# Kernel tuning notes

Hardware: AMD Instinct MI355X
Metric: run time of the kernel (lower is better)

Reference implementation:

```python
import jax, jax.numpy as jnp
import numpy as np

EPS = 1e-5
DN = ('NCHW', 'OIHW', 'NCHW')

def _conv(x, w):
    return jax.lax.conv_general_dilated(x, w, (1, 1), 'VALID', dimension_numbers=DN)

def _bn4(x, g, b, m, v):
    # BatchNorm2d in eval mode, per-channel over NCHW
    inv = g / jnp.sqrt(v + EPS)
    return x * inv[None, :, None, None] + (b - m * inv)[None, :, None, None]

def _bn1(x, g, b, m, v):
    inv = g / jnp.sqrt(v + EPS)
    return x * inv[None, :] + (b - m * inv)[None, :]

def _hardtanh(x):
    return jnp.clip(x, -1.0, 1.0)

def _sign(x):
    return jnp.sign(x)

def _maxpool2(x):
    return jax.lax.reduce_window(x, -jnp.inf, jax.lax.max,
                                 (1, 1, 2, 2), (1, 1, 2, 2), 'VALID')

def setup_inputs() -> dict:
    key = jax.random.key(0)
    ks = jax.random.split(key, 20)
    B = 8192
    d = {
        'x': jax.random.normal(ks[0], (B, 8, 16, 16), jnp.float32),
        'w0': jax.random.normal(ks[1], (32, 8, 3, 3), jnp.float32) * 0.1,
        'b0': jax.random.normal(ks[2], (32,), jnp.float32) * 0.1,
        'g1': jax.random.uniform(ks[3], (32,), jnp.float32, 0.5, 1.5),
        'be1': jax.random.normal(ks[4], (32,), jnp.float32) * 0.1,
        'm1': jax.random.normal(ks[5], (32,), jnp.float32) * 0.1,
        'v1': jax.random.uniform(ks[6], (32,), jnp.float32, 0.5, 1.5),
        'w2': jax.random.normal(ks[7], (32, 32, 3, 3), jnp.float32) * 0.1,
        'g2': jax.random.uniform(ks[8], (32,), jnp.float32, 0.5, 1.5),
        'be2': jax.random.normal(ks[9], (32,), jnp.float32) * 0.1,
        'm2': jax.random.normal(ks[10], (32,), jnp.float32) * 0.1,
        'v2': jax.random.uniform(ks[11], (32,), jnp.float32, 0.5, 1.5),
        'w_fc': jax.random.normal(ks[12], (516, 1152), jnp.float32) * 0.03,
        'g3': jax.random.uniform(ks[13], (516,), jnp.float32, 0.5, 1.5),
        'be3': jax.random.normal(ks[14], (516,), jnp.float32) * 0.1,
        'm3': jax.random.normal(ks[15], (516,), jnp.float32) * 0.1,
        'v3': jax.random.uniform(ks[16], (516,), jnp.float32, 0.5, 1.5),
        'w_last': jax.random.normal(ks[17], (10, 516), jnp.float32) * 0.05,
        'b_last': jax.random.normal(ks[18], (10,), jnp.float32) * 0.05,
    }
    return d

def reference(x, w0, b0, g1, be1, m1, v1, w2, g2, be2, m2, v2,
              w_fc, g3, be3, m3, v3, w_last, b_last):
    # initial float conv + BN + Hardtanh
    h = _conv(x, w0) + b0[None, :, None, None]          # [B,32,14,14]
    h = _hardtanh(_bn4(h, g1, be1, m1, v1))
    # binarized conv (sign(input), sign(weight), no bias)
    h = _conv(_sign(h), _sign(w2))                      # [B,32,12,12]
    h = _hardtanh(_bn4(h, g2, be2, m2, v2))
    h = _maxpool2(h)                                    # [B,32,6,6]
    # dropout is identity in eval mode
    h = h.reshape(h.shape[0], -1)                       # [B,1152]
    # binarized linear (no bias)
    h = _sign(h) @ _sign(w_fc).T                        # [B,516]
    h = _hardtanh(_bn1(h, g3, be3, m3, v3))
    return h @ w_last.T + b_last[None, :]               # [B,10]
```

## Files before the change

### kernel.cpp

```cpp
#include <hip/hip_runtime.h>
#include <cstdint>

#define EPSF 1e-5f

typedef __attribute__((ext_vector_type(8))) short short8;
typedef __attribute__((ext_vector_type(4))) float f32x4;
typedef __attribute__((ext_vector_type(4))) unsigned int u32x4;

__device__ inline uint32_t bf16rne(float x) {
    uint32_t u = __builtin_bit_cast(uint32_t, x);
    return (u + 0x7fffu + ((u >> 16) & 1u)) >> 16;
}
__device__ inline float bf16f(uint32_t b) {
    return __builtin_bit_cast(float, b << 16);
}

__global__ __launch_bounds__(256) void prep_kernel(
    const float* __restrict__ w2, const float* __restrict__ wfc,
    const float* __restrict__ g3, const float* __restrict__ be3,
    const float* __restrict__ m3, const float* __restrict__ v3,
    const float* __restrict__ wlast,
    const float* __restrict__ w0, const float* __restrict__ b0,
    const float* __restrict__ g1, const float* __restrict__ be1,
    const float* __restrict__ m1, const float* __restrict__ v1,
    const float* __restrict__ g2, const float* __restrict__ be2,
    const float* __restrict__ m2, const float* __restrict__ v2,
    uint32_t* __restrict__ w2bits, uint32_t* __restrict__ wfcb,
    float* __restrict__ inv3p, float* __restrict__ sh3p, float* __restrict__ wlt,
    uint32_t* __restrict__ bfrag, float2* __restrict__ bn1c,
    float2* __restrict__ bn1r, int* __restrict__ ti2)
{
    int id = blockIdx.x * 256 + threadIdx.x;
    if (id < 288) {
        int co = id / 9, r = id % 9;
        uint32_t b = 0;
        for (int ci = 0; ci < 32; ci++)
            b |= (uint32_t)(w2[(co * 32 + ci) * 9 + r] < 0.f) << ci;
        w2bits[id] = b;
        return;
    }
    id -= 288;
    if (id < 36 * 576) {
        int j = id / 36, pos = id % 36;
        uint32_t b = 0;
        if (j < 516) {
            const float* row = wfc + j * 1152 + pos;
            for (int c = 0; c < 32; c++)
                b |= (uint32_t)(row[c * 36] < 0.f) << c;
        }
        wfcb[pos * 576 + j] = b;
        return;
    }
    id -= 36 * 576;
    if (id < 576) {
        float iv = 0.f, sh = 0.f;
        if (id < 516) {
            iv = g3[id] / sqrtf(__fadd_rn(v3[id], EPSF));
            sh = __fsub_rn(be3[id], __fmul_rn(m3[id], iv));
        }
        inv3p[id] = iv; sh3p[id] = sh;
        return;
    }
    id -= 576;
    if (id < 5760) {
        int k = id / 576, j = id % 576;
        wlt[id] = (j < 516) ? wlast[k * 516 + j] : 0.f;
        return;
    }
    id -= 5760;
    if (id < 768) {
        int L = id / 12, r = id % 12;
        int nt = r / 6, s = (r % 6) / 2, h = r & 1;
        int g = L >> 4, n = L & 15;
        int tap = 4 * s + g;
        uint32_t d[4] = {0, 0, 0, 0};
        if (tap < 9) {
            int co = nt * 16 + n;
            for (int j2 = 0; j2 < 4; j2++) {
                float wa = w0[co * 72 + (2 * j2) * 9 + tap];
                float wb = w0[co * 72 + (2 * j2 + 1) * 9 + tap];
                uint32_t ha = bf16rne(wa), hb = bf16rne(wb);
                uint32_t va, vb;
                if (h == 0) { va = ha; vb = hb; }
                else { va = bf16rne(wa - bf16f(ha)); vb = bf16rne(wb - bf16f(hb)); }
                d[j2] = va | (vb << 16);
            }
        }
        *(u32x4*)(bfrag + id * 4) = (u32x4){d[0], d[1], d[2], d[3]};
        return;
    }
    id -= 768;
    if (id < 32) {
        float iv = g1[id] / sqrtf(__fadd_rn(v1[id], EPSF));
        float sh = __fsub_rn(be1[id], __fmul_rn(m1[id], iv));
        float off = __fadd_rn(__fmul_rn(b0[id], iv), sh);
        double thrd = -(double)off / (double)iv;
        float thr = (float)thrd;
        float mm = (float)(3.2e-4 / (double)iv + fabs(thrd) * 2e-7 + 1e-9);
        bn1c[id] = make_float2(thr, mm);
        bn1r[id] = make_float2(iv, off);
        return;
    }
    id -= 32;
    if (id < 32) {
        float ivv = g2[id] / sqrtf(__fadd_rn(v2[id], EPSF));
        float shv = __fsub_rn(be2[id], __fmul_rn(m2[id], ivv));
        int M = -290;
        for (int mx = -288; mx <= 288; mx += 2)
            if (__fadd_rn(__fmul_rn((float)mx, ivv), shv) < 0.f) M = mx;
        ti2[id] = (288 - M) >> 1;
    }
}

__device__ __noinline__ bool recheck_sign(const float* __restrict__ xim,
                                          const float* __restrict__ w0,
                                          int py, int px, int co,
                                          const float2* __restrict__ bn1r)
{
    double ad = 0.0;
    for (int ci = 0; ci < 8; ci++)
        for (int ky = 0; ky < 3; ky++)
            for (int kx = 0; kx < 3; kx++)
                ad = fma((double)xim[ci * 256 + (py + ky) * 16 + px + kx],
                         (double)w0[co * 72 + ci * 9 + ky * 3 + kx], ad);
    float2 cc = bn1r[co];
    return (ad * (double)cc.x + (double)cc.y) < 0.0;
}

__global__ __launch_bounds__(128, 4) void convAB(
    const float* __restrict__ x, const float* __restrict__ w0,
    const uint32_t* __restrict__ bfrag, const float2* __restrict__ bn1c,
    const float2* __restrict__ bn1r,
    const uint32_t* __restrict__ w2bits, const int* __restrict__ ti2,
    uint32_t* __restrict__ fcin)
{
    __shared__ __align__(16) char simg[9216];
    __shared__ __align__(8) uint32_t s1l[196];

    const int t = threadIdx.x;
    const int wv = t >> 6, lane = t & 63;
    const int img = blockIdx.x;
    const float* xim = x + img * 2048;
    char* hib = simg;
    char* lob = simg + 4608;

    const int g = lane >> 4;
    const int n = lane & 15;

    short8 Bh[2][3], Bl[2][3];
    {
        const uint32_t* bb = bfrag + lane * 48;
        #pragma unroll
        for (int nt = 0; nt < 2; nt++)
            #pragma unroll
            for (int s = 0; s < 3; s++) {
                Bh[nt][s] = *(const short8*)(bb + (nt * 6 + s * 2) * 4);
                Bl[nt][s] = *(const short8*)(bb + (nt * 6 + s * 2 + 1) * 4);
            }
    }
    const float2 bnA = bn1c[n], bnB = bn1c[16 + n];

    #pragma unroll
    for (int qq = 0; qq < 2; qq++) {
        int pos = lane + 64 * (2 * wv + qq);
        uint32_t hw[4], lw[4];
        #pragma unroll
        for (int j2 = 0; j2 < 4; j2++) {
            float a = xim[(2 * j2) * 256 + pos];
            float b = xim[(2 * j2 + 1) * 256 + pos];
            uint32_t ha = bf16rne(a), hb = bf16rne(b);
            uint32_t la = bf16rne(a - bf16f(ha)), lb = bf16rne(b - bf16f(hb));
            hw[j2] = ha | (hb << 16);
            lw[j2] = la | (lb << 16);
        }
        *(u32x4*)(hib + pos * 16) = (u32x4){hw[0], hw[1], hw[2], hw[3]};
        *(u32x4*)(lob + pos * 16) = (u32x4){lw[0], lw[1], lw[2], lw[3]};
    }
    if (lane < 32) {
        char* gp = (wv == 0) ? hib : lob;
        *(u32x4*)(gp + (256 + lane) * 16) = (u32x4){0, 0, 0, 0};
    }

    int koff[3];
    #pragma unroll
    for (int s = 0; s < 3; s++) {
        int tap = 4 * s + g;
        koff[s] = (tap < 9) ? ((tap / 3) * 16 + (tap % 3)) * 16 : 0;
    }

    __syncthreads();

    for (int tile = wv; tile < 13; tile += 2) {
        int posA = tile * 16 + n;
        int pyA = posA / 14, pxA = posA - pyA * 14;
        int sl = (pyA * 16 + pxA) * 16;

        f32x4 acc0 = {0.f, 0.f, 0.f, 0.f}, acc1 = {0.f, 0.f, 0.f, 0.f};
        #pragma unroll
        for (int s = 0; s < 3; s++) {
            short8 Ah = *(const short8*)(hib + sl + koff[s]);
            short8 Al = *(const short8*)(lob + sl + koff[s]);
            acc0 = __builtin_amdgcn_mfma_f32_16x16x32_bf16(Al, Bh[0][s], acc0, 0, 0, 0);
            acc0 = __builtin_amdgcn_mfma_f32_16x16x32_bf16(Ah, Bl[0][s], acc0, 0, 0, 0);
            acc0 = __builtin_amdgcn_mfma_f32_16x16x32_bf16(Ah, Bh[0][s], acc0, 0, 0, 0);
            acc1 = __builtin_amdgcn_mfma_f32_16x16x32_bf16(Al, Bh[1][s], acc1, 0, 0, 0);
            acc1 = __builtin_amdgcn_mfma_f32_16x16x32_bf16(Ah, Bl[1][s], acc1, 0, 0, 0);
            acc1 = __builtin_amdgcn_mfma_f32_16x16x32_bf16(Ah, Bh[1][s], acc1, 0, 0, 0);
        }

        #pragma unroll
        for (int r = 0; r < 4; r++) {
            int pos = tile * 16 + 4 * g + r;
            float d0 = acc0[r] - bnA.x;
            float d1 = acc1[r] - bnB.x;
            bool bit0, bit1;
            if (__builtin_expect(pos < 196 && fabsf(d0) < bnA.y, 0)) {
                int py = pos / 14, px = pos - py * 14;
                bit0 = recheck_sign(xim, w0, py, px, n, bn1r);
            } else bit0 = (d0 < 0.f);
            if (__builtin_expect(pos < 196 && fabsf(d1) < bnB.y, 0)) {
                int py = pos / 14, px = pos - py * 14;
                bit1 = recheck_sign(xim, w0, py, px, 16 + n, bn1r);
            } else bit1 = (d1 < 0.f);
            unsigned long long m0 = __ballot(bit0);
            unsigned long long m1 = __ballot(bit1);
            uint32_t word = (uint32_t)((m0 >> (16 * g)) & 0xffffull)
                          | ((uint32_t)((m1 >> (16 * g)) & 0xffffull) << 16);
            if (n == 0 && pos < 196) s1l[pos] = word;
        }
    }

    __syncthreads();

    {
        const int c = lane & 31, h = lane >> 5;
        uint32_t wr[9];
        #pragma unroll
        for (int k = 0; k < 9; k++) wr[k] = w2bits[c * 9 + k];
        const int ti = ti2[c];
        uint32_t* outp = fcin + img * 36;
        const int cb0 = 6 * h;

        for (int yy = 0; yy < 3; yy++) {
            const int y2 = 3 * wv + yy;
            const int rbase = 2 * y2 * 14;
            uint32_t win[4][4];
            #pragma unroll
            for (int rr = 0; rr < 4; rr++) {
                uint2 a = *(const uint2*)&s1l[rbase + rr * 14 + cb0];
                uint2 b = *(const uint2*)&s1l[rbase + rr * 14 + cb0 + 2];
                win[rr][0] = a.x; win[rr][1] = a.y; win[rr][2] = b.x; win[rr][3] = b.y;
            }
            for (int step = 0; step < 3; step++) {
                if (step > 0) {
                    #pragma unroll
                    for (int rr = 0; rr < 4; rr++) {
                        win[rr][0] = win[rr][2]; win[rr][1] = win[rr][3];
                        uint2 b = *(const uint2*)&s1l[rbase + rr * 14 + cb0 + 2 * step + 2];
                        win[rr][2] = b.x; win[rr][3] = b.y;
                    }
                }
                int mn = 10000;
                #pragma unroll
                for (int dy = 0; dy < 2; dy++)
                    #pragma unroll
                    for (int dx = 0; dx < 2; dx++) {
                        int p = 0;
                        #pragma unroll
                        for (int ky = 0; ky < 3; ky++)
                            #pragma unroll
                            for (int kx = 0; kx < 3; kx++)
                                p += __popc(win[dy + ky][dx + kx] ^ wr[ky * 3 + kx]);
                        mn = min(mn, p);
                    }
                unsigned long long mb = __ballot(mn >= ti);
                if (lane == 0)  outp[y2 * 6 + step]     = (uint32_t)mb;
                if (lane == 32) outp[y2 * 6 + step + 3] = (uint32_t)(mb >> 32);
            }
        }
    }
}

__global__ __launch_bounds__(256) void fcC(
    const uint32_t* __restrict__ fcin, const uint32_t* __restrict__ wfcb,
    const float* __restrict__ inv3p, const float* __restrict__ sh3p,
    const float* __restrict__ wlt, const float* __restrict__ blast,
    float* __restrict__ out)
{
    __shared__ uint32_t l_in[288];
    const int t = threadIdx.x, wid = t >> 6, lane = t & 63;

    for (int i = t; i < 288; i += 256) l_in[i] = fcin[blockIdx.x * 288 + i];
    __syncthreads();

    const int b0i = blockIdx.x * 8 + wid * 2;
    const uint32_t* in0 = &l_in[wid * 72];

    int pc0[9], pc1[9];
    #pragma unroll
    for (int q = 0; q < 9; q++) { pc0[q] = 0; pc1[q] = 0; }

    for (int w = 0; w < 36; w++) {
        uint32_t i0 = in0[w], i1 = in0[36 + w];
        const uint32_t* wf = wfcb + w * 576 + lane;
        #pragma unroll
        for (int q = 0; q < 9; q++) {
            uint32_t f = wf[q * 64];
            pc0[q] += __popc(i0 ^ f);
            pc1[q] += __popc(i1 ^ f);
        }
    }

    float oa[2][10];
    #pragma unroll
    for (int b = 0; b < 2; b++)
        #pragma unroll
        for (int k = 0; k < 10; k++) oa[b][k] = 0.f;

    #pragma unroll
    for (int q = 0; q < 9; q++) {
        int j = lane + 64 * q;
        float ivv = inv3p[j], shv = sh3p[j];
        float t0 = fminf(1.f, fmaxf(-1.f, __fadd_rn(__fmul_rn((float)(1152 - 2 * pc0[q]), ivv), shv)));
        float t1 = fminf(1.f, fmaxf(-1.f, __fadd_rn(__fmul_rn((float)(1152 - 2 * pc1[q]), ivv), shv)));
        #pragma unroll
        for (int k = 0; k < 10; k++) {
            float wv = wlt[k * 576 + j];
            oa[0][k] = fmaf(t0, wv, oa[0][k]);
            oa[1][k] = fmaf(t1, wv, oa[1][k]);
        }
    }

    #pragma unroll
    for (int m = 1; m < 64; m <<= 1)
        #pragma unroll
        for (int b = 0; b < 2; b++)
            #pragma unroll
            for (int k = 0; k < 10; k++)
                oa[b][k] += __shfl_xor(oa[b][k], m, 64);

    if (lane == 0) {
        for (int b = 0; b < 2; b++)
            for (int k = 0; k < 10; k++)
                out[(b0i + b) * 10 + k] = oa[b][k] + blast[k];
    }
}

extern "C" void kernel_launch(void* const* d_in, const int* in_sizes, int n_in,
                              void* d_out, int out_size, void* d_ws, size_t ws_size,
                              hipStream_t stream)
{
    (void)in_sizes; (void)n_in; (void)out_size; (void)ws_size;
    const float* x     = (const float*)d_in[0];
    const float* w0    = (const float*)d_in[1];
    const float* b0    = (const float*)d_in[2];
    const float* g1    = (const float*)d_in[3];
    const float* be1   = (const float*)d_in[4];
    const float* m1    = (const float*)d_in[5];
    const float* v1    = (const float*)d_in[6];
    const float* w2    = (const float*)d_in[7];
    const float* g2    = (const float*)d_in[8];
    const float* be2   = (const float*)d_in[9];
    const float* m2    = (const float*)d_in[10];
    const float* v2    = (const float*)d_in[11];
    const float* wfc   = (const float*)d_in[12];
    const float* g3    = (const float*)d_in[13];
    const float* be3   = (const float*)d_in[14];
    const float* m3    = (const float*)d_in[15];
    const float* v3    = (const float*)d_in[16];
    const float* wlast = (const float*)d_in[17];
    const float* blast = (const float*)d_in[18];

    char* ws = (char*)d_ws;
    uint32_t* fcin   = (uint32_t*)(ws + 6422528);
    uint32_t* w2bits = (uint32_t*)(ws + 7602176);
    uint32_t* wfcb   = (uint32_t*)(ws + 7603328);
    float*    inv3p  = (float*)(ws + 7686272);
    float*    sh3p   = (float*)(ws + 7688576);
    float*    wlt    = (float*)(ws + 7690880);
    uint32_t* bfrag  = (uint32_t*)(ws + 7713920);
    float2*   bn1c   = (float2*)(ws + 7726208);
    float2*   bn1r   = (float2*)(ws + 7726464);
    int*      ti2    = (int*)(ws + 7726720);

    prep_kernel<<<111, 256, 0, stream>>>(w2, wfc, g3, be3, m3, v3, wlast,
                                         w0, b0, g1, be1, m1, v1,
                                         g2, be2, m2, v2,
                                         w2bits, wfcb, inv3p, sh3p, wlt,
                                         bfrag, bn1c, bn1r, ti2);
    convAB<<<8192, 128, 0, stream>>>(x, w0, bfrag, bn1c, bn1r,
                                     w2bits, ti2, fcin);
    fcC<<<1024, 256, 0, stream>>>(fcin, wfcb, inv3p, sh3p, wlt, blast, (float*)d_out);
}
```

Baseline: 218.7 us.

## Fuse binarized FC and final linear layer into conv kernel

Removes the separate fcC kernel and computes the binarized FC, BN/hardtanh and the last linear layer inside the per-image conv block. The packed FC input bits stay in shared memory instead of going through a global workspace, and one kernel launch is dropped. In exchange, each block processes a single image, so the FC weight matrix and the last-layer weights are re-read from cache once per image rather than being shared across several images. The two waves split the output-neuron chunks and combine their results through shared memory with an extra barrier.

```diff
diff --git a/kernel.cpp b/kernel.cpp
--- a/kernel.cpp
+++ b/kernel.cpp
@@ -127,15 +127,20 @@
     return (ad * (double)cc.x + (double)cc.y) < 0.0;
 }
 
-__global__ __launch_bounds__(128, 4) void convAB(
+__global__ __launch_bounds__(128, 4) void convABC(
     const float* __restrict__ x, const float* __restrict__ w0,
     const uint32_t* __restrict__ bfrag, const float2* __restrict__ bn1c,
     const float2* __restrict__ bn1r,
     const uint32_t* __restrict__ w2bits, const int* __restrict__ ti2,
-    uint32_t* __restrict__ fcin)
+    const uint32_t* __restrict__ wfcb,
+    const float* __restrict__ inv3p, const float* __restrict__ sh3p,
+    const float* __restrict__ wlt, const float* __restrict__ blast,
+    float* __restrict__ out)
 {
     __shared__ __align__(16) char simg[9216];
     __shared__ __align__(8) uint32_t s1l[196];
+    __shared__ __align__(8) uint32_t fcw[36];
+    __shared__ float ored[2][10];
 
     const int t = threadIdx.x;
     const int wv = t >> 6, lane = t & 63;
@@ -238,7 +243,6 @@
         #pragma unroll
         for (int k = 0; k < 9; k++) wr[k] = w2bits[c * 9 + k];
         const int ti = ti2[c];
-        uint32_t* outp = fcin + img * 36;
         const int cb0 = 6 * h;
 
         for (int yy = 0; yy < 3; yy++) {
@@ -274,76 +278,65 @@
                         mn = min(mn, p);
                     }
                 unsigned long long mb = __ballot(mn >= ti);
-                if (lane == 0)  outp[y2 * 6 + step]     = (uint32_t)mb;
-                if (lane == 32) outp[y2 * 6 + step + 3] = (uint32_t)(mb >> 32);
-            }
-        }
-    }
-}
-
-__global__ __launch_bounds__(256) void fcC(
-    const uint32_t* __restrict__ fcin, const uint32_t* __restrict__ wfcb,
-    const float* __restrict__ inv3p, const float* __restrict__ sh3p,
-    const float* __restrict__ wlt, const float* __restrict__ blast,
-    float* __restrict__ out)
-{
-    __shared__ uint32_t l_in[288];
-    const int t = threadIdx.x, wid = t >> 6, lane = t & 63;
-
-    for (int i = t; i < 288; i += 256) l_in[i] = fcin[blockIdx.x * 288 + i];
+                if (lane == 0)  fcw[y2 * 6 + step]     = (uint32_t)mb;
+                if (lane == 32) fcw[y2 * 6 + step + 3] = (uint32_t)(mb >> 32);
+            }
+        }
+    }
+
     __syncthreads();
 
-    const int b0i = blockIdx.x * 8 + wid * 2;
-    const uint32_t* in0 = &l_in[wid * 72];
-
-    int pc0[9], pc1[9];
-    #pragma unroll
-    for (int q = 0; q < 9; q++) { pc0[q] = 0; pc1[q] = 0; }
-
-    for (int w = 0; w < 36; w++) {
-        uint32_t i0 = in0[w], i1 = in0[36 + w];
-        const uint32_t* wf = wfcb + w * 576 + lane;
-        #pragma unroll
-        for (int q = 0; q < 9; q++) {
-            uint32_t f = wf[q * 64];
-            pc0[q] += __popc(i0 ^ f);
-            pc1[q] += __popc(i1 ^ f);
-        }
-    }
-
-    float oa[2][10];
-    #pragma unroll
-    for (int b = 0; b < 2; b++)
-        #pragma unroll
-        for (int k = 0; k < 10; k++) oa[b][k] = 0.f;
-
-    #pragma unroll
-    for (int q = 0; q < 9; q++) {
-        int j = lane + 64 * q;
-        float ivv = inv3p[j], shv = sh3p[j];
-        float t0 = fminf(1.f, fmaxf(-1.f, __fadd_rn(__fmul_rn((float)(1152 - 2 * pc0[q]), ivv), shv)));
-        float t1 = fminf(1.f, fmaxf(-1.f, __fadd_rn(__fmul_rn((float)(1152 - 2 * pc1[q]), ivv), shv)));
-        #pragma unroll
-        for (int k = 0; k < 10; k++) {
-            float wv = wlt[k * 576 + j];
-            oa[0][k] = fmaf(t0, wv, oa[0][k]);
-            oa[1][k] = fmaf(t1, wv, oa[1][k]);
-        }
-    }
-
-    #pragma unroll
-    for (int m = 1; m < 64; m <<= 1)
-        #pragma unroll
-        for (int b = 0; b < 2; b++)
+    {
+        const int q0 = wv * 5;
+        int pc[5];
+        #pragma unroll
+        for (int qq = 0; qq < 5; qq++) pc[qq] = 0;
+
+        for (int w = 0; w < 36; w++) {
+            uint32_t iw = fcw[w];
+            const uint32_t* wf = wfcb + w * 576 + lane;
+            #pragma unroll
+            for (int qq = 0; qq < 5; qq++) {
+                if (q0 + qq < 9) {
+                    uint32_t f = wf[(q0 + qq) * 64];
+                    pc[qq] += __popc(iw ^ f);
+                }
+            }
+        }
+
+        float oa[10];
+        #pragma unroll
+        for (int k = 0; k < 10; k++) oa[k] = 0.f;
+
+        #pragma unroll
+        for (int qq = 0; qq < 5; qq++) {
+            if (q0 + qq < 9) {
+                int j = lane + 64 * (q0 + qq);
+                float ivv = inv3p[j], shv = sh3p[j];
+                float tv = fminf(1.f, fmaxf(-1.f,
+                    __fadd_rn(__fmul_rn((float)(1152 - 2 * pc[qq]), ivv), shv)));
+                #pragma unroll
+                for (int k = 0; k < 10; k++) {
+                    float wvv = wlt[k * 576 + j];
+                    oa[k] = fmaf(tv, wvv, oa[k]);
+                }
+            }
+        }
+
+        #pragma unroll
+        for (int m = 1; m < 64; m <<= 1)
             #pragma unroll
             for (int k = 0; k < 10; k++)
-                oa[b][k] += __shfl_xor(oa[b][k], m, 64);
-
-    if (lane == 0) {
-        for (int b = 0; b < 2; b++)
-            for (int k = 0; k < 10; k++)
-                out[(b0i + b) * 10 + k] = oa[b][k] + blast[k];
-    }
+                oa[k] += __shfl_xor(oa[k], m, 64);
+
+        if (lane == 0)
+            #pragma unroll
+            for (int k = 0; k < 10; k++) ored[wv][k] = oa[k];
+    }
+
+    __syncthreads();
+    if (t < 10)
+        out[img * 10 + t] = (ored[0][t] + ored[1][t]) + blast[t];
 }
 
 extern "C" void kernel_launch(void* const* d_in, const int* in_sizes, int n_in,
@@ -372,7 +365,6 @@
     const float* blast = (const float*)d_in[18];
 
     char* ws = (char*)d_ws;
-    uint32_t* fcin   = (uint32_t*)(ws + 6422528);
     uint32_t* w2bits = (uint32_t*)(ws + 7602176);
     uint32_t* wfcb   = (uint32_t*)(ws + 7603328);
     float*    inv3p  = (float*)(ws + 7686272);
@@ -388,7 +380,8 @@
                                          g2, be2, m2, v2,
                                          w2bits, wfcb, inv3p, sh3p, wlt,
                                          bfrag, bn1c, bn1r, ti2);
-    convAB<<<8192, 128, 0, stream>>>(x, w0, bfrag, bn1c, bn1r,
-                                     w2bits, ti2, fcin);
-    fcC<<<1024, 256, 0, stream>>>(fcin, wfcb, inv3p, sh3p, wlt, blast, (float*)d_out);
-}
+    convABC<<<8192, 128, 0, stream>>>(x, w0, bfrag, bn1c, bn1r,
+                                      w2bits, ti2, wfcb,
+                                      inv3p, sh3p, wlt, blast,
+                                      (float*)d_out);
+}
```

Result: slower. 303.4 us (+38.8%).
